# Optimization experiments

Measured on AMD Instinct MI355X. Metric: run time of the kernel, lower is better.

Reference implementation:

```python
import jax, jax.numpy as jnp
import numpy as np

HEAD_DIM = 64  # config['head_dim']
# dropout_prob=0.1 is a no-op in eval mode; reference computes deterministic attention.

def setup_inputs() -> dict:
    key = jax.random.key(0)
    kq, kk, kv = jax.random.split(key, 3)
    shape = (2, 12, 2048, HEAD_DIM)  # [batch, heads, seq, head_dim]
    Q = jax.random.normal(kq, shape, dtype=jnp.float32)
    K = jax.random.normal(kk, shape, dtype=jnp.float32)
    V = jax.random.normal(kv, shape, dtype=jnp.float32)
    return {"Q": Q, "K": K, "V": V}

def reference(Q, K, V):
    # dot = Q @ K^T / sqrt(head_dim); attn = softmax(dot); X = attn @ V
    scale = 1.0 / np.float32(np.sqrt(HEAD_DIM))
    dot = jnp.einsum('bhqd,bhkd->bhqk', Q, K) * scale  # [B,H,S,S]
    attn = jax.nn.softmax(dot, axis=-1)
    X = jnp.einsum('bhqk,bhkd->bhqd', attn, V)
    return X
```

## Files before the change

### kernel.cpp

```cpp
#include <hip/hip_runtime.h>
#include <hip/hip_bf16.h>

typedef __attribute__((ext_vector_type(8))) short bf16x8;
typedef __attribute__((ext_vector_type(4))) float f32x4;
typedef __attribute__((ext_vector_type(4))) unsigned short u16x4;
typedef __attribute__((ext_vector_type(2))) unsigned int u32x2;
typedef __attribute__((ext_vector_type(4))) unsigned int u32x4;
typedef __attribute__((ext_vector_type(4))) _Float16 f16x4;
typedef __attribute__((ext_vector_type(8))) _Float16 f16x8;
typedef __attribute__((ext_vector_type(2))) __fp16 h16x2;
typedef __attribute__((ext_vector_type(4))) __fp16 h16x4;

#define SEQ 2048
#define HD 64
#define BH 24

__device__ __forceinline__ unsigned bfpack(float a, float b) {
  union { float f; unsigned u; } ua, ub; ua.f = a; ub.f = b;
  return __builtin_amdgcn_perm(ub.u + 0x8000u, ua.u + 0x8000u, 0x07060302u);
}
__device__ __forceinline__ unsigned short f2bf(float f) {
  union { float f; unsigned u; } v; v.f = f;
  unsigned r = v.u + 0x7fffu + ((v.u >> 16) & 1u);
  return (unsigned short)(r >> 16);
}

__global__ __launch_bounds__(256) void prep_kv(const float* __restrict__ K,
                                               const float* __restrict__ V,
                                               unsigned* __restrict__ Kb,
                                               _Float16* __restrict__ Vt) {
  __shared__ _Float16 t[64 * 68];
  const int bh = blockIdx.y;
  const int k0 = blockIdx.x * 64;
  const int tid = threadIdx.x;

  const float4* ks = (const float4*)(K + ((size_t)bh * SEQ + k0) * HD);
  unsigned* kd = Kb + ((size_t)bh * SEQ + k0) * (HD / 2);
#pragma unroll
  for (int i = 0; i < 4; ++i) {
    int f = tid + i * 256;
    float4 v = ks[f];
    u32x2 o;
    o.x = bfpack(v.x, v.y);
    o.y = bfpack(v.z, v.w);
    *(u32x2*)&kd[f * 2] = o;
  }

  const float4* vs = (const float4*)(V + ((size_t)bh * SEQ + k0) * HD);
#pragma unroll
  for (int i = 0; i < 4; ++i) {
    int f = tid + i * 256;
    int k = f >> 4, cg = f & 15;
    float4 v = vs[k * 16 + cg];
    int dg = cg * 4;
    t[(dg + 0) * 68 + k] = (_Float16)v.x;
    t[(dg + 1) * 68 + k] = (_Float16)v.y;
    t[(dg + 2) * 68 + k] = (_Float16)v.z;
    t[(dg + 3) * 68 + k] = (_Float16)v.w;
  }
  __syncthreads();
  int d = tid >> 2, kg = (tid & 3) * 16;
  _Float16* g = Vt + ((size_t)(bh * 64 + d)) * SEQ + k0 + (kg & 32) + ((kg >> 4) & 1) * 4;
#pragma unroll
  for (int r = 0; r < 4; ++r) {
    f16x4 x = *(f16x4*)&t[d * 68 + kg + r * 4];
    *(f16x4*)&g[r * 8] = x;
  }
}

__global__ __launch_bounds__(256) void attn_main(const float* __restrict__ Q,
                                                 const unsigned short* __restrict__ Kb,
                                                 const _Float16* __restrict__ Vt,
                                                 float* __restrict__ O) {
  __shared__ unsigned short kv[3][8192];

  const int tid  = threadIdx.x;
  const int lane = tid & 63;
  const int wv   = tid >> 6;
  const int quad = lane >> 4;
  const int n    = lane & 15;

  const int bh = blockIdx.x;
  const int q0 = blockIdx.y * 64;

  const float qscale = 0.125f * 1.44269504088896f;

  bf16x8 qf[2];
  {
    const float* qb = Q + ((size_t)bh * SEQ + q0 + wv * 16 + n) * HD;
#pragma unroll
    for (int h = 0; h < 2; ++h) {
      float4 a = *(const float4*)(qb + h * 32 + quad * 8);
      float4 b = *(const float4*)(qb + h * 32 + quad * 8 + 4);
      u32x4 pk;
      pk.x = bfpack(a.x * qscale, a.y * qscale);
      pk.y = bfpack(a.z * qscale, a.w * qscale);
      pk.z = bfpack(b.x * qscale, b.y * qscale);
      pk.w = bfpack(b.z * qscale, b.w * qscale);
      qf[h] = __builtin_bit_cast(bf16x8, pk);
    }
  }

  const unsigned short* Kbase = Kb + (size_t)bh * SEQ * HD;
  const unsigned short* Vbase = (const unsigned short*)(Vt + (size_t)bh * HD * SEQ);
  const unsigned short* ksrc[2];
  const unsigned short* vsrc[2];
  int soff[2];
#pragma unroll
  for (int i = 0; i < 2; ++i) {
    int s = i * 256 + tid;
    int r = s >> 3, p = s & 7, G = p ^ (r & 7);
    ksrc[i] = Kbase + r * HD + G * 8;
    vsrc[i] = Vbase + (size_t)r * SEQ + G * 8;
    soff[i] = s * 8;
  }

#define DMA_TO(buf_, it_)                                                                 \
  {                                                                                       \
    unsigned short* db_ = &kv[buf_][0];                                                   \
    _Pragma("unroll")                                                                     \
    for (int i_ = 0; i_ < 2; ++i_) {                                                      \
      __builtin_amdgcn_global_load_lds(                                                   \
          (const __attribute__((address_space(1))) void*)(ksrc[i_] + (size_t)(it_) * 4096), \
          (__attribute__((address_space(3))) void*)(db_ + soff[i_]), 16, 0, 0);           \
      __builtin_amdgcn_global_load_lds(                                                   \
          (const __attribute__((address_space(1))) void*)(vsrc[i_] + (size_t)(it_) * 64), \
          (__attribute__((address_space(3))) void*)(db_ + 4096 + soff[i_]), 16, 0, 0);    \
    }                                                                                     \
    asm volatile("" ::: "memory");                      \
  }

  f32x4 o[4] = {{0,0,0,0},{0,0,0,0},{0,0,0,0},{0,0,0,0}};
  float lsum = 0.f;

  int ro[2];
#pragma unroll
  for (int h = 0; h < 2; ++h) ro[h] = n * 64 + (((h * 4 + quad) ^ (n & 7)) * 8);

#define COMPUTE(buf_)                                                                     \
  {                                                                                       \
    const unsigned short* kb = &kv[buf_][0];                                              \
    const unsigned short* vb = kb + 4096;                                                 \
    f32x4 s[4] = {{0,0,0,0},{0,0,0,0},{0,0,0,0},{0,0,0,0}};                               \
    _Pragma("unroll")                                                                     \
    for (int t = 0; t < 4; ++t) {                                                         \
      _Pragma("unroll")                                                                   \
      for (int h = 0; h < 2; ++h) {                                                       \
        bf16x8 a = *(const bf16x8*)&kb[t * 1024 + ro[h]];                                 \
        s[t] = __builtin_amdgcn_mfma_f32_16x16x32_bf16(a, qf[h], s[t], 0, 0, 0);          \
      }                                                                                   \
    }                                                                                     \
    f16x4 pf[4];                                                                          \
    _Pragma("unroll")                                                                     \
    for (int c = 0; c < 4; ++c) {                                                         \
      float e0 = __builtin_amdgcn_exp2f(s[c][0]);                                         \
      float e1 = __builtin_amdgcn_exp2f(s[c][1]);                                         \
      float e2 = __builtin_amdgcn_exp2f(s[c][2]);                                         \
      float e3 = __builtin_amdgcn_exp2f(s[c][3]);                                         \
      lsum += (e0 + e1) + (e2 + e3);                                                      \
      h16x2 a_ = __builtin_amdgcn_cvt_pkrtz(e0, e1);                                      \
      h16x2 b_ = __builtin_amdgcn_cvt_pkrtz(e2, e3);                                      \
      h16x4 ab_ = __builtin_shufflevector(a_, b_, 0, 1, 2, 3);                            \
      pf[c] = __builtin_bit_cast(f16x4, ab_);                                             \
    }                                                                                     \
    _Pragma("unroll")                                                                     \
    for (int t = 0; t < 4; ++t) {                                                         \
      _Pragma("unroll")                                                                   \
      for (int h = 0; h < 2; ++h) {                                                       \
        f16x8 v8 = *(const f16x8*)((const _Float16*)&vb[t * 1024 + ro[h]]);               \
        f16x4 vlo = __builtin_shufflevector(v8, v8, 0, 1, 2, 3);                          \
        f16x4 vhi = __builtin_shufflevector(v8, v8, 4, 5, 6, 7);                          \
        o[t] = __builtin_amdgcn_mfma_f32_16x16x16f16(vlo, pf[2 * h], o[t], 0, 0, 0);      \
        o[t] = __builtin_amdgcn_mfma_f32_16x16x16f16(vhi, pf[2 * h + 1], o[t], 0, 0, 0);  \
      }                                                                                   \
    }                                                                                     \
  }

  DMA_TO(0, 0);
  DMA_TO(1, 1);

  int bc = 0;
  int bd = 2;
  for (int it = 0; it < 31; ++it) {
    asm volatile("s_waitcnt vmcnt(4)\n\ts_barrier" ::: "memory");
    if (it < 30) DMA_TO(bd, it + 2);
    COMPUTE(bc);
    bc = (bc == 2) ? 0 : bc + 1;
    bd = (bd == 2) ? 0 : bd + 1;
  }
  asm volatile("s_waitcnt vmcnt(0)\n\ts_barrier" ::: "memory");
  COMPUTE(bc);

#undef DMA_TO
#undef COMPUTE

  {
    float l = lsum;
    l += __shfl_xor(l, 16);
    l += __shfl_xor(l, 32);
    float inv = 1.0f / l;
    float* og = O + ((size_t)bh * SEQ + q0 + wv * 16 + n) * HD + quad * 4;
#pragma unroll
    for (int t = 0; t < 4; ++t) {
      f32x4 r = o[t];
      r.x *= inv; r.y *= inv; r.z *= inv; r.w *= inv;
      *(f32x4*)(og + t * 16) = r;
    }
  }
}

#define F_QT 128
#define F_KT 64
#define F_LD 72

__global__ __launch_bounds__(512) void attn_fwd(const float* __restrict__ Q,
                                                const float* __restrict__ K,
                                                const float* __restrict__ V,
                                                float* __restrict__ O) {
  __shared__ unsigned short sm[(F_QT + F_KT + HD + 8 * 16) * F_LD];
  unsigned short* Qs = sm;
  unsigned short* Ks = Qs + F_QT * F_LD;
  unsigned short* Vt = Ks + F_KT * F_LD;
  unsigned short* Ps = Vt + HD * F_LD;

  const int tid = threadIdx.x, lane = tid & 63, wv = tid >> 6;
  const int quad = lane >> 4, n = lane & 15;
  const int bh = blockIdx.y, q0 = blockIdx.x * F_QT;
  const float* Qg = Q + ((size_t)bh * SEQ + q0) * HD;
  const float* Kg = K + (size_t)bh * SEQ * HD;
  const float* Vg = V + (size_t)bh * SEQ * HD;
  float* Og = O + ((size_t)bh * SEQ + q0) * HD;
  const float qscale = 0.125f * 1.44269504088896f;

#pragma unroll
  for (int i = 0; i < 4; ++i) {
    int f = tid + i * 512;
    int row = f >> 4, cg = f & 15;
    float4 qv = ((const float4*)Qg)[row * 16 + cg];
    u16x4 h;
    h.x = f2bf(qv.x * qscale); h.y = f2bf(qv.y * qscale);
    h.z = f2bf(qv.z * qscale); h.w = f2bf(qv.w * qscale);
    *(u16x4*)&Qs[row * F_LD + cg * 4] = h;
  }
  __syncthreads();
  bf16x8 qf0 = *(const bf16x8*)&Qs[(wv * 16 + n) * F_LD + quad * 8];
  bf16x8 qf1 = *(const bf16x8*)&Qs[(wv * 16 + n) * F_LD + 32 + quad * 8];
  f32x4 o[4] = {{0,0,0,0},{0,0,0,0},{0,0,0,0},{0,0,0,0}};
  float mrow[4] = {-1e30f,-1e30f,-1e30f,-1e30f};
  float lrow[4] = {0.f,0.f,0.f,0.f};
  unsigned short* Pw = Ps + wv * 16 * F_LD;

  for (int it = 0; it < SEQ / F_KT; ++it) {
    __syncthreads();
    const float* Ktg = Kg + (size_t)it * F_KT * HD;
    const float* Vtg = Vg + (size_t)it * F_KT * HD;
#pragma unroll
    for (int i = 0; i < 2; ++i) {
      int f = tid + i * 512;
      int row = f >> 4, cg = f & 15;
      float4 kvv = ((const float4*)Ktg)[row * 16 + cg];
      u16x4 hk;
      hk.x = f2bf(kvv.x); hk.y = f2bf(kvv.y); hk.z = f2bf(kvv.z); hk.w = f2bf(kvv.w);
      *(u16x4*)&Ks[row * F_LD + cg * 4] = hk;
      float4 vv = ((const float4*)Vtg)[row * 16 + cg];
      Vt[(cg * 4 + 0) * F_LD + row] = f2bf(vv.x);
      Vt[(cg * 4 + 1) * F_LD + row] = f2bf(vv.y);
      Vt[(cg * 4 + 2) * F_LD + row] = f2bf(vv.z);
      Vt[(cg * 4 + 3) * F_LD + row] = f2bf(vv.w);
    }
    __syncthreads();
    f32x4 s[4];
#pragma unroll
    for (int t = 0; t < 4; ++t) {
      bf16x8 b0 = *(const bf16x8*)&Ks[(t * 16 + n) * F_LD + quad * 8];
      bf16x8 b1 = *(const bf16x8*)&Ks[(t * 16 + n) * F_LD + 32 + quad * 8];
      f32x4 c = {0,0,0,0};
      c = __builtin_amdgcn_mfma_f32_16x16x32_bf16(qf0, b0, c, 0, 0, 0);
      c = __builtin_amdgcn_mfma_f32_16x16x32_bf16(qf1, b1, c, 0, 0, 0);
      s[t] = c;
    }
    float mnew[4], alpha[4], rsum[4];
#pragma unroll
    for (int r = 0; r < 4; ++r) {
      float ml = fmaxf(fmaxf(s[0][r], s[1][r]), fmaxf(s[2][r], s[3][r]));
      ml = fmaxf(ml, __shfl_xor(ml, 1));
      ml = fmaxf(ml, __shfl_xor(ml, 2));
      ml = fmaxf(ml, __shfl_xor(ml, 4));
      ml = fmaxf(ml, __shfl_xor(ml, 8));
      mnew[r] = fmaxf(mrow[r], ml);
      alpha[r] = __builtin_amdgcn_exp2f(mrow[r] - mnew[r]);
      mrow[r] = mnew[r];
      rsum[r] = 0.f;
    }
#pragma unroll
    for (int t = 0; t < 4; ++t)
#pragma unroll
      for (int r = 0; r < 4; ++r) {
        float p = __builtin_amdgcn_exp2f(s[t][r] - mnew[r]);
        rsum[r] += p;
        Pw[(quad * 4 + r) * F_LD + t * 16 + n] = f2bf(p);
      }
#pragma unroll
    for (int r = 0; r < 4; ++r) {
      float rs = rsum[r];
      rs += __shfl_xor(rs, 1); rs += __shfl_xor(rs, 2);
      rs += __shfl_xor(rs, 4); rs += __shfl_xor(rs, 8);
      lrow[r] = lrow[r] * alpha[r] + rs;
      o[0][r] *= alpha[r]; o[1][r] *= alpha[r];
      o[2][r] *= alpha[r]; o[3][r] *= alpha[r];
    }
    asm volatile("s_waitcnt lgkmcnt(0)" ::: "memory");
    bf16x8 p0 = *(const bf16x8*)&Pw[n * F_LD + quad * 8];
    bf16x8 p1 = *(const bf16x8*)&Pw[n * F_LD + 32 + quad * 8];
#pragma unroll
    for (int t = 0; t < 4; ++t) {
      bf16x8 v0 = *(const bf16x8*)&Vt[(t * 16 + n) * F_LD + quad * 8];
      bf16x8 v1 = *(const bf16x8*)&Vt[(t * 16 + n) * F_LD + 32 + quad * 8];
      o[t] = __builtin_amdgcn_mfma_f32_16x16x32_bf16(p0, v0, o[t], 0, 0, 0);
      o[t] = __builtin_amdgcn_mfma_f32_16x16x32_bf16(p1, v1, o[t], 0, 0, 0);
    }
  }
  float inv[4];
#pragma unroll
  for (int r = 0; r < 4; ++r) inv[r] = 1.0f / lrow[r];
#pragma unroll
  for (int t = 0; t < 4; ++t)
#pragma unroll
    for (int r = 0; r < 4; ++r)
      Og[(wv * 16 + quad * 4 + r) * HD + t * 16 + n] = o[t][r] * inv[r];
}

extern "C" void kernel_launch(void* const* d_in, const int* in_sizes, int n_in,
                              void* d_out, int out_size, void* d_ws, size_t ws_size,
                              hipStream_t stream) {
  const float* Q = (const float*)d_in[0];
  const float* K = (const float*)d_in[1];
  const float* V = (const float*)d_in[2];
  float* O = (float*)d_out;

  const size_t mat = (size_t)BH * SEQ * HD;
  const size_t need = 2 * mat * sizeof(unsigned short);

  if (ws_size >= need) {
    unsigned short* Kb = (unsigned short*)d_ws;
    _Float16* Vt = (_Float16*)(Kb + mat);
    prep_kv<<<dim3(SEQ / 64, BH), 256, 0, stream>>>(K, V, (unsigned*)Kb, Vt);
    attn_main<<<dim3(BH, SEQ / 64), 256, 0, stream>>>(Q, Kb, Vt, O);
  } else {
    attn_fwd<<<dim3(SEQ / F_QT, BH), 512, 0, stream>>>(Q, K, V, O);
  }
}
```

Baseline: 122.9 us.

## Split key tile across waves with cross-wave LDS reduction of partial outputs

```diff
diff --git a/kernel.cpp b/kernel.cpp
--- a/kernel.cpp
+++ b/kernel.cpp
@@ -60,23 +60,23 @@
   }
   __syncthreads();
   int d = tid >> 2, kg = (tid & 3) * 16;
-  _Float16* g = Vt + ((size_t)(bh * 64 + d)) * SEQ + k0 + (kg & 32) + ((kg >> 4) & 1) * 4;
+  _Float16* g = Vt + ((size_t)(bh * 64 + d)) * SEQ + k0 + kg;
 #pragma unroll
   for (int r = 0; r < 4; ++r) {
     f16x4 x = *(f16x4*)&t[d * 68 + kg + r * 4];
-    *(f16x4*)&g[r * 8] = x;
-  }
-}
-
-__global__ __launch_bounds__(256) void attn_main(const float* __restrict__ Q,
-                                                 const unsigned short* __restrict__ Kb,
-                                                 const _Float16* __restrict__ Vt,
-                                                 float* __restrict__ O) {
+    *(f16x4*)&g[r * 4] = x;
+  }
+}
+
+__global__ __launch_bounds__(256, 3) void attn_main(const float* __restrict__ Q,
+                                                    const unsigned short* __restrict__ Kb,
+                                                    const _Float16* __restrict__ Vt,
+                                                    float* __restrict__ O) {
   __shared__ unsigned short kv[3][8192];
 
   const int tid  = threadIdx.x;
   const int lane = tid & 63;
-  const int wv   = tid >> 6;
+  const int w    = tid >> 6;
   const int quad = lane >> 4;
   const int n    = lane & 15;
 
@@ -85,9 +85,10 @@
 
   const float qscale = 0.125f * 1.44269504088896f;
 
-  bf16x8 qf[2];
-  {
-    const float* qb = Q + ((size_t)bh * SEQ + q0 + wv * 16 + n) * HD;
+  bf16x8 qf[4][2];
+#pragma unroll
+  for (int u = 0; u < 4; ++u) {
+    const float* qb = Q + ((size_t)bh * SEQ + q0 + u * 16 + n) * HD;
 #pragma unroll
     for (int h = 0; h < 2; ++h) {
       float4 a = *(const float4*)(qb + h * 32 + quad * 8);
@@ -97,7 +98,7 @@
       pk.y = bfpack(a.z * qscale, a.w * qscale);
       pk.z = bfpack(b.x * qscale, b.y * qscale);
       pk.w = bfpack(b.z * qscale, b.w * qscale);
-      qf[h] = __builtin_bit_cast(bf16x8, pk);
+      qf[u][h] = __builtin_bit_cast(bf16x8, pk);
     }
   }
 
@@ -127,15 +128,23 @@
           (const __attribute__((address_space(1))) void*)(vsrc[i_] + (size_t)(it_) * 64), \
           (__attribute__((address_space(3))) void*)(db_ + 4096 + soff[i_]), 16, 0, 0);    \
     }                                                                                     \
-    asm volatile("" ::: "memory");                      \
-  }
-
-  f32x4 o[4] = {{0,0,0,0},{0,0,0,0},{0,0,0,0},{0,0,0,0}};
-  float lsum = 0.f;
+    asm volatile("" ::: "memory");                                                        \
+  }
+
+  f32x4 o[4][4];
+#pragma unroll
+  for (int dt = 0; dt < 4; ++dt)
+#pragma unroll
+    for (int u = 0; u < 4; ++u) o[dt][u] = (f32x4){0.f, 0.f, 0.f, 0.f};
+  float lsum[4] = {0.f, 0.f, 0.f, 0.f};
 
   int ro[2];
 #pragma unroll
   for (int h = 0; h < 2; ++h) ro[h] = n * 64 + (((h * 4 + quad) ^ (n & 7)) * 8);
+  int vo[4];
+#pragma unroll
+  for (int dt = 0; dt < 4; ++dt)
+    vo[dt] = dt * 1024 + n * 64 + (((w * 2 + (quad >> 1)) ^ (n & 7)) * 8) + (quad & 1) * 4;
 
 #define COMPUTE(buf_)                                                                     \
   {                                                                                       \
@@ -143,36 +152,31 @@
     const unsigned short* vb = kb + 4096;                                                 \
     f32x4 s[4] = {{0,0,0,0},{0,0,0,0},{0,0,0,0},{0,0,0,0}};                               \
     _Pragma("unroll")                                                                     \
-    for (int t = 0; t < 4; ++t) {                                                         \
+    for (int h = 0; h < 2; ++h) {                                                         \
+      bf16x8 a = *(const bf16x8*)&kb[w * 1024 + ro[h]];                                   \
       _Pragma("unroll")                                                                   \
-      for (int h = 0; h < 2; ++h) {                                                       \
-        bf16x8 a = *(const bf16x8*)&kb[t * 1024 + ro[h]];                                 \
-        s[t] = __builtin_amdgcn_mfma_f32_16x16x32_bf16(a, qf[h], s[t], 0, 0, 0);          \
-      }                                                                                   \
+      for (int u = 0; u < 4; ++u)                                                         \
+        s[u] = __builtin_amdgcn_mfma_f32_16x16x32_bf16(a, qf[u][h], s[u], 0, 0, 0);       \
     }                                                                                     \
     f16x4 pf[4];                                                                          \
     _Pragma("unroll")                                                                     \
-    for (int c = 0; c < 4; ++c) {                                                         \
-      float e0 = __builtin_amdgcn_exp2f(s[c][0]);                                         \
-      float e1 = __builtin_amdgcn_exp2f(s[c][1]);                                         \
-      float e2 = __builtin_amdgcn_exp2f(s[c][2]);                                         \
-      float e3 = __builtin_amdgcn_exp2f(s[c][3]);                                         \
-      lsum += (e0 + e1) + (e2 + e3);                                                      \
+    for (int u = 0; u < 4; ++u) {                                                         \
+      float e0 = __builtin_amdgcn_exp2f(s[u][0]);                                         \
+      float e1 = __builtin_amdgcn_exp2f(s[u][1]);                                         \
+      float e2 = __builtin_amdgcn_exp2f(s[u][2]);                                         \
+      float e3 = __builtin_amdgcn_exp2f(s[u][3]);                                         \
+      lsum[u] += (e0 + e1) + (e2 + e3);                                                   \
       h16x2 a_ = __builtin_amdgcn_cvt_pkrtz(e0, e1);                                      \
       h16x2 b_ = __builtin_amdgcn_cvt_pkrtz(e2, e3);                                      \
       h16x4 ab_ = __builtin_shufflevector(a_, b_, 0, 1, 2, 3);                            \
-      pf[c] = __builtin_bit_cast(f16x4, ab_);                                             \
+      pf[u] = __builtin_bit_cast(f16x4, ab_);                                             \
     }                                                                                     \
     _Pragma("unroll")                                                                     \
-    for (int t = 0; t < 4; ++t) {                                                         \
+    for (int dt = 0; dt < 4; ++dt) {                                                      \
+      f16x4 vf = *(const f16x4*)((const _Float16*)vb + vo[dt]);                           \
       _Pragma("unroll")                                                                   \
-      for (int h = 0; h < 2; ++h) {                                                       \
-        f16x8 v8 = *(const f16x8*)((const _Float16*)&vb[t * 1024 + ro[h]]);               \
-        f16x4 vlo = __builtin_shufflevector(v8, v8, 0, 1, 2, 3);                          \
-        f16x4 vhi = __builtin_shufflevector(v8, v8, 4, 5, 6, 7);                          \
-        o[t] = __builtin_amdgcn_mfma_f32_16x16x16f16(vlo, pf[2 * h], o[t], 0, 0, 0);      \
-        o[t] = __builtin_amdgcn_mfma_f32_16x16x16f16(vhi, pf[2 * h + 1], o[t], 0, 0, 0);  \
-      }                                                                                   \
+      for (int u = 0; u < 4; ++u)                                                         \
+        o[dt][u] = __builtin_amdgcn_mfma_f32_16x16x16f16(vf, pf[u], o[dt][u], 0, 0, 0);   \
     }                                                                                     \
   }
 
@@ -194,17 +198,64 @@
 #undef DMA_TO
 #undef COMPUTE
 
-  {
-    float l = lsum;
-    l += __shfl_xor(l, 16);
-    l += __shfl_xor(l, 32);
-    float inv = 1.0f / l;
-    float* og = O + ((size_t)bh * SEQ + q0 + wv * 16 + n) * HD + quad * 4;
-#pragma unroll
-    for (int t = 0; t < 4; ++t) {
-      f32x4 r = o[t];
-      r.x *= inv; r.y *= inv; r.z *= inv; r.w *= inv;
-      *(f32x4*)(og + t * 16) = r;
+#pragma unroll
+  for (int u = 0; u < 4; ++u) {
+    lsum[u] += __shfl_xor(lsum[u], 16);
+    lsum[u] += __shfl_xor(lsum[u], 32);
+  }
+
+  float* red = (float*)&kv[0][0];
+  float* lred = red + 2 * 4096;
+
+  __syncthreads();
+  if (w & 1) {
+    int s = w >> 1;
+#pragma unroll
+    for (int dt = 0; dt < 4; ++dt)
+#pragma unroll
+      for (int u = 0; u < 4; ++u)
+        *(f32x4*)&red[s * 4096 + (dt * 4 + u) * 256 + lane * 4] = o[dt][u];
+#pragma unroll
+    for (int u = 0; u < 4; ++u) lred[s * 256 + u * 64 + lane] = lsum[u];
+  }
+  __syncthreads();
+  if (!(w & 1)) {
+    int s = w >> 1;
+#pragma unroll
+    for (int dt = 0; dt < 4; ++dt)
+#pragma unroll
+      for (int u = 0; u < 4; ++u)
+        o[dt][u] += *(f32x4*)&red[s * 4096 + (dt * 4 + u) * 256 + lane * 4];
+#pragma unroll
+    for (int u = 0; u < 4; ++u) lsum[u] += lred[s * 256 + u * 64 + lane];
+  }
+  __syncthreads();
+  if (w == 2) {
+#pragma unroll
+    for (int dt = 0; dt < 4; ++dt)
+#pragma unroll
+      for (int u = 0; u < 4; ++u)
+        *(f32x4*)&red[4096 + (dt * 4 + u) * 256 + lane * 4] = o[dt][u];
+#pragma unroll
+    for (int u = 0; u < 4; ++u) lred[256 + u * 64 + lane] = lsum[u];
+  }
+  __syncthreads();
+  if (w == 0) {
+#pragma unroll
+    for (int dt = 0; dt < 4; ++dt)
+#pragma unroll
+      for (int u = 0; u < 4; ++u)
+        o[dt][u] += *(f32x4*)&red[4096 + (dt * 4 + u) * 256 + lane * 4];
+#pragma unroll
+    for (int u = 0; u < 4; ++u) {
+      float inv = 1.0f / (lsum[u] + lred[256 + u * 64 + lane]);
+      float* og = O + ((size_t)bh * SEQ + q0 + u * 16 + n) * HD + quad * 4;
+#pragma unroll
+      for (int dt = 0; dt < 4; ++dt) {
+        f32x4 r = o[dt][u];
+        r.x *= inv; r.y *= inv; r.z *= inv; r.w *= inv;
+        *(f32x4*)(og + dt * 16) = r;
+      }
     }
   }
 }
```

Result: faster. 119.5 us (-2.8%).
